# Kernel optimization log

Measured on AMD Instinct MI355X. Metric: run time of the kernel, lower is better.

## Reference

```python
import jax, jax.numpy as jnp
import numpy as np

N_SLOTS = 24   # n_slots from __init__
N_ITERS = 25   # fixed Lloyd iterations (stand-in for sklearn max_iter/convergence)
NORM_EPS = 1e-12  # torch F.normalize eps


def setup_inputs() -> dict:
    key = jax.random.key(0)
    features = jax.random.normal(key, (32, 4096, 256), dtype=jnp.float32)
    return {"features": features}


def _pairwise_sqdist(x, x_sq, centers):
    # x: [B,N,D], x_sq: [B,N,1], centers: [B,K,D] -> [B,N,K]
    c_sq = jnp.sum(centers * centers, axis=-1)  # [B,K]
    return x_sq - 2.0 * jnp.einsum('bnd,bkd->bnk', x, centers) + c_sq[:, None, :]


def _kmeans_batched(x, k, n_iters):
    # x: [B,N,D] -> centers [B,K,D], assignments [B,N]
    B, N, D = x.shape
    # deterministic init: K evenly-spaced points per batch item
    init_idx = jnp.linspace(0, N - 1, k).astype(jnp.int32)
    centers0 = x[:, init_idx, :]  # [B,K,D]
    x_sq = jnp.sum(x * x, axis=-1, keepdims=True)  # [B,N,1]

    def step(centers, _):
        d = _pairwise_sqdist(x, x_sq, centers)          # [B,N,K]
        assign = jnp.argmin(d, axis=-1)                 # [B,N]
        onehot = jax.nn.one_hot(assign, k, dtype=x.dtype)  # [B,N,K]
        counts = jnp.sum(onehot, axis=1)                # [B,K]
        sums = jnp.einsum('bnk,bnd->bkd', onehot, x)    # [B,K,D] scatter-mean numerator
        new_centers = sums / jnp.maximum(counts, 1.0)[..., None]
        # empty clusters keep their previous center
        new_centers = jnp.where(counts[..., None] > 0, new_centers, centers)
        return new_centers, None

    centers, _ = jax.lax.scan(step, centers0, None, length=n_iters)
    final_assign = jnp.argmin(_pairwise_sqdist(x, x_sq, centers), axis=-1)
    return centers, final_assign


def reference(features):
    # L2-normalize along feature dim (use_l2_normalization=True)
    norm = jnp.sqrt(jnp.sum(features * features, axis=-1, keepdims=True))
    f = features / jnp.maximum(norm, NORM_EPS)
    # original detaches before clustering (sklearn on CPU): no gradient flow
    f = jax.lax.stop_gradient(f)
    centers, assign = _kmeans_batched(f, N_SLOTS, N_ITERS)
    # slot masks: one_hot then transpose(-2,-1) -> [B, K, N] float32
    slot_masks = jax.nn.one_hot(assign, N_SLOTS, dtype=jnp.float32).transpose(0, 2, 1)
    return centers, slot_masks
```

## Files before the change

### kernel.cpp

```cpp
#include <hip/hip_runtime.h>
#include <math.h>


#define BATCH 32
#define NPTS 4096
#define DIM 256
#define NSLOT 24
#define NITER 25
#define NCH 16
#define CPTS 256

__global__ __launch_bounds__(256) void k_norm(const float* __restrict__ feat,
                                              double* __restrict__ inv_norm) {
  int lane = threadIdx.x & 63;
  int wid = threadIdx.x >> 6;
  int p = blockIdx.x * 4 + wid;
  const float4 v = *(const float4*)(feat + (size_t)p * DIM + lane * 4);
  double s = (double)v.x * v.x + (double)v.y * v.y + (double)v.z * v.z + (double)v.w * v.w;
#pragma unroll
  for (int m = 32; m; m >>= 1) s += __shfl_xor(s, m);
  if (lane == 0) inv_norm[p] = 1.0 / fmax(sqrt(s), 1e-12);
}

__device__ __forceinline__ double block_sum_256(double v, double* red) {
#pragma unroll
  for (int m = 32; m; m >>= 1) v += __shfl_xor(v, m);
  int w = threadIdx.x >> 6;
  if ((threadIdx.x & 63) == 0) red[w] = v;
  __syncthreads();
  return red[0] + red[1] + red[2] + red[3];
}

__global__ __launch_bounds__(256) void k_init_centers(const float* __restrict__ feat,
                                                      const double* __restrict__ inv_norm,
                                                      double* __restrict__ centers,
                                                      float* __restrict__ cT32,
                                                      float* __restrict__ c_sq32) {
  __shared__ double red[4];
  int t = threadIdx.x, k = blockIdx.x, b = blockIdx.y;
  int idx = (int)((double)k * (NPTS - 1) / (NSLOT - 1));
  double v = (double)feat[((size_t)b * NPTS + idx) * DIM + t] * inv_norm[b * NPTS + idx];
  centers[((size_t)b * NSLOT + k) * DIM + t] = v;
  cT32[((size_t)b * DIM + t) * NSLOT + k] = (float)v;
  double s = block_sum_256(v * v, red);
  if (t == 0) c_sq32[b * NSLOT + k] = (float)s;
}

__global__ __launch_bounds__(256) void k_transpose(const float* __restrict__ feat,
                                                   float* __restrict__ xT) {
  __shared__ float tile[64][65];
  int ix = threadIdx.x & 63, iy = threadIdx.x >> 6;
  int bx = blockIdx.x, by = blockIdx.y, b = blockIdx.z;
  const float* fb = feat + ((size_t)b * NPTS + bx * 64) * DIM + by * 64;
#pragma unroll
  for (int r = 0; r < 64; r += 4)
    tile[r + iy][ix] = fb[(size_t)(r + iy) * DIM + ix];
  __syncthreads();
  float* xb = xT + ((size_t)b * DIM + by * 64) * NPTS + bx * 64;
#pragma unroll
  for (int r = 0; r < 64; r += 4)
    xb[(size_t)(r + iy) * NPTS + ix] = tile[ix][r + iy];
}

template <bool USE_T>
__global__ __launch_bounds__(256) void k_assign(const float* __restrict__ feat,
                                                const float* __restrict__ xT,
                                                const double* __restrict__ inv_norm,
                                                const float* __restrict__ cT32,
                                                const float* __restrict__ c_sq32,
                                                int* __restrict__ assign) {
  __shared__ float part[3][64][NSLOT + 1];
  int lane = threadIdx.x & 63;
  int q = __builtin_amdgcn_readfirstlane(threadIdx.x >> 6);
  int blk = blockIdx.x, b = blockIdx.y;
  int n = blk * 64 + lane;
  const float* cb = cT32 + ((size_t)b * DIM + q * 64) * NSLOT;

  float dot[NSLOT];
#pragma unroll
  for (int k = 0; k < NSLOT; ++k) dot[k] = 0.0f;

  for (int d = 0; d < 64; d += 8) {
    float x[8];
    if (USE_T) {
      const float* xp = xT + ((size_t)b * DIM + q * 64 + d) * NPTS + n;
#pragma unroll
      for (int j = 0; j < 8; ++j) x[j] = xp[(size_t)j * NPTS];
    } else {
      float4 v = *(const float4*)(feat + ((size_t)b * NPTS + n) * DIM + q * 64 + d);
      float4 u = *(const float4*)(feat + ((size_t)b * NPTS + n) * DIM + q * 64 + d + 4);
      x[0] = v.x; x[1] = v.y; x[2] = v.z; x[3] = v.w;
      x[4] = u.x; x[5] = u.y; x[6] = u.z; x[7] = u.w;
    }
    const float* cp = cb + (size_t)d * NSLOT;
#pragma unroll
    for (int k = 0; k < NSLOT; ++k) {
      float s = dot[k];
#pragma unroll
      for (int j = 0; j < 8; ++j) s = fmaf(x[j], cp[j * NSLOT + k], s);
      dot[k] = s;
    }
  }

  if (q) {
#pragma unroll
    for (int k = 0; k < NSLOT; ++k) part[q - 1][lane][k] = dot[k];
  }
  __syncthreads();

  if (q == 0) {
    float inv = (float)inv_norm[b * NPTS + n];
    const float* csq = c_sq32 + b * NSLOT;
    int a = 0;
    float best = 0.0f;
#pragma unroll
    for (int k = 0; k < NSLOT; ++k) {
      float df = dot[k] + part[0][lane][k] + part[1][lane][k] + part[2][lane][k];
      float s = csq[k] - 2.0f * (df * inv);
      if (k == 0) { best = s; }
      else if (s < best) { best = s; a = k; }
    }
    assign[b * NPTS + n] = a;
  }
}

__global__ __launch_bounds__(256) void k_clusterS(const float* __restrict__ feat,
                                                  const double* __restrict__ inv_norm,
                                                  const int* __restrict__ assign,
                                                  double* __restrict__ psumG) {
  __shared__ double part[NSLOT * DIM];
  __shared__ int a_lds[CPTS];
  __shared__ double i_lds[CPTS];
  int t = threadIdx.x, ch = blockIdx.x, b = blockIdx.y;

  a_lds[t] = assign[b * NPTS + ch * CPTS + t];
  i_lds[t] = inv_norm[b * NPTS + ch * CPTS + t];
#pragma unroll
  for (int i = 0; i < NSLOT; ++i) part[i * DIM + t] = 0.0;
  __syncthreads();

  const float* fb = feat + ((size_t)b * NPTS + ch * CPTS) * DIM + t;
  for (int row = 0; row < CPTS; row += 4) {
    float x0 = fb[(size_t)(row + 0) * DIM];
    float x1 = fb[(size_t)(row + 1) * DIM];
    float x2 = fb[(size_t)(row + 2) * DIM];
    float x3 = fb[(size_t)(row + 3) * DIM];
    int a0 = __builtin_amdgcn_readfirstlane(a_lds[row + 0]);
    int a1 = __builtin_amdgcn_readfirstlane(a_lds[row + 1]);
    int a2 = __builtin_amdgcn_readfirstlane(a_lds[row + 2]);
    int a3 = __builtin_amdgcn_readfirstlane(a_lds[row + 3]);
    double v0 = (double)x0 * i_lds[row + 0];
    double v1 = (double)x1 * i_lds[row + 1];
    double v2 = (double)x2 * i_lds[row + 2];
    double v3 = (double)x3 * i_lds[row + 3];
    part[a0 * DIM + t] += v0;
    part[a1 * DIM + t] += v1;
    part[a2 * DIM + t] += v2;
    part[a3 * DIM + t] += v3;
  }
  __syncthreads();

  double* ps = psumG + (size_t)(b * NCH + ch) * NSLOT * DIM;
#pragma unroll
  for (int i = 0; i < NSLOT; ++i) ps[i * DIM + t] = part[i * DIM + t];
}

__global__ __launch_bounds__(256) void k_upd3(const double* __restrict__ psumG,
                                              const int* __restrict__ assign,
                                              double* __restrict__ centers,
                                              float* __restrict__ cT32,
                                              float* __restrict__ c_sq32) {
  __shared__ double red[4];
  __shared__ int scnt;
  int t = threadIdx.x, k = blockIdx.x, b = blockIdx.y;
  if (t == 0) scnt = 0;
  __syncthreads();

  double s = 0.0;
#pragma unroll
  for (int ch = 0; ch < NCH; ++ch)
    s += psumG[((size_t)(b * NCH + ch) * NSLOT + k) * DIM + t];

  int c_loc = 0;
  const int* ab = assign + b * NPTS;
#pragma unroll
  for (int j = 0; j < NPTS / 256; ++j) c_loc += (ab[t + j * 256] == k) ? 1 : 0;
#pragma unroll
  for (int m = 32; m; m >>= 1) c_loc += __shfl_xor(c_loc, m);
  if ((t & 63) == 0) atomicAdd(&scnt, c_loc);
  __syncthreads();
  int cnt = scnt;

  size_t ci = ((size_t)b * NSLOT + k) * DIM + t;
  double nc = (cnt > 0) ? (s / (double)cnt) : centers[ci];
  centers[ci] = nc;
  cT32[((size_t)b * DIM + t) * NSLOT + k] = (float)nc;
  double sq = block_sum_256(nc * nc, red);
  if (t == 0) c_sq32[b * NSLOT + k] = (float)sq;
}

__global__ __launch_bounds__(256) void k_mask(const int* __restrict__ assign,
                                              float* __restrict__ masks) {
  int t = threadIdx.x, nc = blockIdx.x, k = blockIdx.y, b = blockIdx.z;
  int n = nc * 256 + t;
  masks[((size_t)b * NSLOT + k) * NPTS + n] = (assign[b * NPTS + n] == k) ? 1.0f : 0.0f;
}

__global__ __launch_bounds__(256) void k_copyc(const double* __restrict__ centers,
                                               float* __restrict__ out_centers) {
  int t = threadIdx.x, k = blockIdx.x, b = blockIdx.y;
  size_t i = ((size_t)b * NSLOT + k) * DIM + t;
  out_centers[i] = (float)centers[i];
}

extern "C" void kernel_launch(void* const* d_in, const int* in_sizes, int n_in,
                              void* d_out, int out_size, void* d_ws, size_t ws_size,
                              hipStream_t stream) {
  (void)in_sizes; (void)n_in; (void)out_size;
  const float* feat = (const float*)d_in[0];
  float* out_centers = (float*)d_out;
  float* out_masks = out_centers + (size_t)BATCH * NSLOT * DIM;

  char* ws = (char*)d_ws;
  double* inv_norm = (double*)ws; ws += (size_t)BATCH * NPTS * 8;
  double* centers  = (double*)ws; ws += (size_t)BATCH * NSLOT * DIM * 8;
  float* cT32      = (float*)ws;  ws += (size_t)BATCH * DIM * NSLOT * 4;
  float* c_sq32    = (float*)ws;  ws += (size_t)BATCH * NSLOT * 4;
  int* assign      = (int*)ws;    ws += (size_t)BATCH * NPTS * 4;
  double* psumG    = (double*)ws; ws += (size_t)BATCH * NCH * NSLOT * DIM * 8;
  float* xT        = (float*)ws;
  size_t need_xT = (size_t)(ws - (char*)d_ws) + (size_t)BATCH * DIM * NPTS * 4;
  bool useT = ws_size >= need_xT;

  k_norm<<<BATCH * NPTS / 4, 256, 0, stream>>>(feat, inv_norm);
  k_init_centers<<<dim3(NSLOT, BATCH), 256, 0, stream>>>(feat, inv_norm, centers,
                                                         cT32, c_sq32);
  if (useT)
    k_transpose<<<dim3(NPTS / 64, DIM / 64, BATCH), 256, 0, stream>>>(feat, xT);

  for (int it = 0; it <= NITER; ++it) {
    if (useT)
      k_assign<true><<<dim3(NPTS / 64, BATCH), 256, 0, stream>>>(feat, xT, inv_norm,
                                                                 cT32, c_sq32, assign);
    else
      k_assign<false><<<dim3(NPTS / 64, BATCH), 256, 0, stream>>>(feat, xT, inv_norm,
                                                                  cT32, c_sq32, assign);
    if (it == NITER) break;
    k_clusterS<<<dim3(NCH, BATCH), 256, 0, stream>>>(feat, inv_norm, assign, psumG);
    k_upd3<<<dim3(NSLOT, BATCH), 256, 0, stream>>>(psumG, assign, centers, cT32, c_sq32);
  }

  k_mask<<<dim3(NPTS / 256, NSLOT, BATCH), 256, 0, stream>>>(assign, out_masks);
  k_copyc<<<dim3(NSLOT, BATCH), 256, 0, stream>>>(centers, out_centers);
}
```

Measured before the change: 2.047 ms.

## Fuse assignment with per-chunk cluster sums via sorted point lists

Merges the assignment and cluster-sum kernels into one kernel per 256-point chunk. Points are bucketed by assigned slot using ballots, then feature rows are summed per slot in a register double accumulator and written to per-chunk partials along with counts. The update kernel reads these counts instead of rescanning assignments, and the final pass writes masks directly. This removes the assign buffer round-trip and one launch per iteration, but uses 4x fewer blocks with each thread computing the full dot product, which lowers occupancy.

```diff
diff --git a/kernel.cpp b/kernel.cpp
--- a/kernel.cpp
+++ b/kernel.cpp
@@ -62,134 +62,153 @@
     xb[(size_t)(r + iy) * NPTS + ix] = tile[ix][r + iy];
 }
 
-template <bool USE_T>
-__global__ __launch_bounds__(256) void k_assign(const float* __restrict__ feat,
-                                                const float* __restrict__ xT,
-                                                const double* __restrict__ inv_norm,
-                                                const float* __restrict__ cT32,
-                                                const float* __restrict__ c_sq32,
-                                                int* __restrict__ assign) {
-  __shared__ float part[3][64][NSLOT + 1];
-  int lane = threadIdx.x & 63;
-  int q = __builtin_amdgcn_readfirstlane(threadIdx.x >> 6);
-  int blk = blockIdx.x, b = blockIdx.y;
-  int n = blk * 64 + lane;
-  const float* cb = cT32 + ((size_t)b * DIM + q * 64) * NSLOT;
-
-  float dot[NSLOT];
-#pragma unroll
-  for (int k = 0; k < NSLOT; ++k) dot[k] = 0.0f;
-
-  for (int d = 0; d < 64; d += 8) {
+template <bool USE_T, bool FINAL>
+__global__ __launch_bounds__(256) void k_fused(const float* __restrict__ feat,
+                                               const float* __restrict__ xT,
+                                               const double* __restrict__ inv_norm,
+                                               const float* __restrict__ cT32,
+                                               const float* __restrict__ c_sq32,
+                                               double* __restrict__ psumG,
+                                               int* __restrict__ cntG,
+                                               float* __restrict__ masks) {
+  __shared__ double i_lds[CPTS];
+  __shared__ int a_lds[CPTS];
+  __shared__ unsigned short list[CPTS];
+  __shared__ unsigned char sk_arr[CPTS];
+  __shared__ int wcnt[4][NSLOT], goff[4][NSLOT];
+  __shared__ int off_lds[NSLOT], tot_lds[NSLOT];
+  int ch = blockIdx.x, b = blockIdx.y;
+  int t = threadIdx.x;
+  int lane = t & 63;
+  int w = __builtin_amdgcn_readfirstlane(t >> 6);
+
+  i_lds[t] = inv_norm[b * NPTS + ch * CPTS + t];
+  __syncthreads();
+
+  const float* cT = cT32 + (size_t)b * DIM * NSLOT;
+  const float* csq = c_sq32 + b * NSLOT;
+  float acc[NSLOT], cur[NSLOT];
+#pragma unroll
+  for (int k = 0; k < NSLOT; ++k) acc[k] = 0.0f;
+  const float* xp = USE_T ? (xT + (size_t)b * DIM * NPTS + ch * CPTS + t)
+                          : (feat + ((size_t)b * NPTS + ch * CPTS + t) * DIM);
+  for (int q = 0; q < 4; ++q) {
+#pragma unroll
+    for (int k = 0; k < NSLOT; ++k) cur[k] = 0.0f;
+    for (int d0 = q * 64; d0 < q * 64 + 64; d0 += 8) {
+      float x[8];
+      if (USE_T) {
+#pragma unroll
+        for (int j = 0; j < 8; ++j) x[j] = xp[(size_t)(d0 + j) * NPTS];
+      } else {
+        float4 v = *(const float4*)(xp + d0);
+        float4 u = *(const float4*)(xp + d0 + 4);
+        x[0] = v.x; x[1] = v.y; x[2] = v.z; x[3] = v.w;
+        x[4] = u.x; x[5] = u.y; x[6] = u.z; x[7] = u.w;
+      }
+      const float* cp = cT + d0 * NSLOT;
+#pragma unroll
+      for (int k = 0; k < NSLOT; ++k) {
+        float s = cur[k];
+#pragma unroll
+        for (int j = 0; j < 8; ++j) s = fmaf(x[j], cp[j * NSLOT + k], s);
+        cur[k] = s;
+      }
+    }
+#pragma unroll
+    for (int k = 0; k < NSLOT; ++k) acc[k] += cur[k];
+  }
+  float inv = (float)i_lds[t];
+  int a = 0;
+  float best = 0.0f;
+#pragma unroll
+  for (int k = 0; k < NSLOT; ++k) {
+    float s = csq[k] - 2.0f * (acc[k] * inv);
+    if (k == 0) { best = s; }
+    else if (s < best) { best = s; a = k; }
+  }
+
+  if (FINAL) {
+#pragma unroll
+    for (int k = 0; k < NSLOT; ++k)
+      masks[((size_t)b * NSLOT + k) * NPTS + ch * CPTS + t] = (a == k) ? 1.0f : 0.0f;
+    return;
+  }
+  a_lds[t] = a;
+  __syncthreads();
+
+  for (int k = 0; k < NSLOT; ++k) {
+    unsigned long long bal = __ballot(a == k);
+    if (lane == 0) wcnt[w][k] = __popcll(bal);
+  }
+  __syncthreads();
+  if (t < NSLOT) {
+    tot_lds[t] = wcnt[0][t] + wcnt[1][t] + wcnt[2][t] + wcnt[3][t];
+  }
+  __syncthreads();
+  if (t < NSLOT) {
+    int off = 0;
+    for (int k2 = 0; k2 < t; ++k2) off += tot_lds[k2];
+    off_lds[t] = off;
+    int base = off;
+#pragma unroll
+    for (int g = 0; g < 4; ++g) { goff[g][t] = base; base += wcnt[g][t]; }
+    cntG[(b * NCH + ch) * NSLOT + t] = tot_lds[t];
+  }
+  __syncthreads();
+  unsigned long long lt = (1ull << lane) - 1ull;
+  for (int k = 0; k < NSLOT; ++k) {
+    unsigned long long bal = __ballot(a == k);
+    if (a == k) {
+      int pos = goff[w][k] + __popcll(bal & lt);
+      list[pos] = (unsigned short)t;
+      sk_arr[pos] = (unsigned char)k;
+    }
+  }
+  __syncthreads();
+
+  const float* fb = feat + ((size_t)b * NPTS + ch * CPTS) * DIM + t;
+  double* psB = psumG + (size_t)(b * NCH + ch) * NSLOT * DIM + t;
+  double racc = 0.0;
+  for (int i0 = 0; i0 < CPTS; i0 += 8) {
+    int nn[8];
     float x[8];
-    if (USE_T) {
-      const float* xp = xT + ((size_t)b * DIM + q * 64 + d) * NPTS + n;
-#pragma unroll
-      for (int j = 0; j < 8; ++j) x[j] = xp[(size_t)j * NPTS];
-    } else {
-      float4 v = *(const float4*)(feat + ((size_t)b * NPTS + n) * DIM + q * 64 + d);
-      float4 u = *(const float4*)(feat + ((size_t)b * NPTS + n) * DIM + q * 64 + d + 4);
-      x[0] = v.x; x[1] = v.y; x[2] = v.z; x[3] = v.w;
-      x[4] = u.x; x[5] = u.y; x[6] = u.z; x[7] = u.w;
+#pragma unroll
+    for (int j = 0; j < 8; ++j)
+      nn[j] = __builtin_amdgcn_readfirstlane((int)list[i0 + j]);
+#pragma unroll
+    for (int j = 0; j < 8; ++j) x[j] = fb[(size_t)nn[j] * DIM];
+#pragma unroll
+    for (int j = 0; j < 8; ++j) {
+      int i = i0 + j;
+      racc += (double)x[j] * i_lds[nn[j]];
+      int kcur = __builtin_amdgcn_readfirstlane((int)sk_arr[i]);
+      int knxt = (i < CPTS - 1) ? __builtin_amdgcn_readfirstlane((int)sk_arr[i + 1]) : -1;
+      if (kcur != knxt) {
+        psB[(size_t)kcur * DIM] = racc;
+        racc = 0.0;
+      }
     }
-    const float* cp = cb + (size_t)d * NSLOT;
-#pragma unroll
-    for (int k = 0; k < NSLOT; ++k) {
-      float s = dot[k];
-#pragma unroll
-      for (int j = 0; j < 8; ++j) s = fmaf(x[j], cp[j * NSLOT + k], s);
-      dot[k] = s;
-    }
-  }
-
-  if (q) {
-#pragma unroll
-    for (int k = 0; k < NSLOT; ++k) part[q - 1][lane][k] = dot[k];
-  }
-  __syncthreads();
-
-  if (q == 0) {
-    float inv = (float)inv_norm[b * NPTS + n];
-    const float* csq = c_sq32 + b * NSLOT;
-    int a = 0;
-    float best = 0.0f;
-#pragma unroll
-    for (int k = 0; k < NSLOT; ++k) {
-      float df = dot[k] + part[0][lane][k] + part[1][lane][k] + part[2][lane][k];
-      float s = csq[k] - 2.0f * (df * inv);
-      if (k == 0) { best = s; }
-      else if (s < best) { best = s; a = k; }
-    }
-    assign[b * NPTS + n] = a;
-  }
-}
-
-__global__ __launch_bounds__(256) void k_clusterS(const float* __restrict__ feat,
-                                                  const double* __restrict__ inv_norm,
-                                                  const int* __restrict__ assign,
-                                                  double* __restrict__ psumG) {
-  __shared__ double part[NSLOT * DIM];
-  __shared__ int a_lds[CPTS];
-  __shared__ double i_lds[CPTS];
-  int t = threadIdx.x, ch = blockIdx.x, b = blockIdx.y;
-
-  a_lds[t] = assign[b * NPTS + ch * CPTS + t];
-  i_lds[t] = inv_norm[b * NPTS + ch * CPTS + t];
-#pragma unroll
-  for (int i = 0; i < NSLOT; ++i) part[i * DIM + t] = 0.0;
-  __syncthreads();
-
-  const float* fb = feat + ((size_t)b * NPTS + ch * CPTS) * DIM + t;
-  for (int row = 0; row < CPTS; row += 4) {
-    float x0 = fb[(size_t)(row + 0) * DIM];
-    float x1 = fb[(size_t)(row + 1) * DIM];
-    float x2 = fb[(size_t)(row + 2) * DIM];
-    float x3 = fb[(size_t)(row + 3) * DIM];
-    int a0 = __builtin_amdgcn_readfirstlane(a_lds[row + 0]);
-    int a1 = __builtin_amdgcn_readfirstlane(a_lds[row + 1]);
-    int a2 = __builtin_amdgcn_readfirstlane(a_lds[row + 2]);
-    int a3 = __builtin_amdgcn_readfirstlane(a_lds[row + 3]);
-    double v0 = (double)x0 * i_lds[row + 0];
-    double v1 = (double)x1 * i_lds[row + 1];
-    double v2 = (double)x2 * i_lds[row + 2];
-    double v3 = (double)x3 * i_lds[row + 3];
-    part[a0 * DIM + t] += v0;
-    part[a1 * DIM + t] += v1;
-    part[a2 * DIM + t] += v2;
-    part[a3 * DIM + t] += v3;
-  }
-  __syncthreads();
-
-  double* ps = psumG + (size_t)(b * NCH + ch) * NSLOT * DIM;
-#pragma unroll
-  for (int i = 0; i < NSLOT; ++i) ps[i * DIM + t] = part[i * DIM + t];
+  }
+  for (int k = 0; k < NSLOT; ++k)
+    if (tot_lds[k] == 0) psB[(size_t)k * DIM] = 0.0;
 }
 
 __global__ __launch_bounds__(256) void k_upd3(const double* __restrict__ psumG,
-                                              const int* __restrict__ assign,
+                                              const int* __restrict__ cntG,
                                               double* __restrict__ centers,
                                               float* __restrict__ cT32,
                                               float* __restrict__ c_sq32) {
   __shared__ double red[4];
-  __shared__ int scnt;
   int t = threadIdx.x, k = blockIdx.x, b = blockIdx.y;
-  if (t == 0) scnt = 0;
-  __syncthreads();
-
   double s = 0.0;
 #pragma unroll
   for (int ch = 0; ch < NCH; ++ch)
     s += psumG[((size_t)(b * NCH + ch) * NSLOT + k) * DIM + t];
-
-  int c_loc = 0;
-  const int* ab = assign + b * NPTS;
-#pragma unroll
-  for (int j = 0; j < NPTS / 256; ++j) c_loc += (ab[t + j * 256] == k) ? 1 : 0;
-#pragma unroll
-  for (int m = 32; m; m >>= 1) c_loc += __shfl_xor(c_loc, m);
-  if ((t & 63) == 0) atomicAdd(&scnt, c_loc);
-  __syncthreads();
-  int cnt = scnt;
+  int cnt = 0;
+#pragma unroll
+  for (int ch = 0; ch < NCH; ++ch)
+    cnt += cntG[(b * NCH + ch) * NSLOT + k];
 
   size_t ci = ((size_t)b * NSLOT + k) * DIM + t;
   double nc = (cnt > 0) ? (s / (double)cnt) : centers[ci];
@@ -197,13 +216,6 @@
   cT32[((size_t)b * DIM + t) * NSLOT + k] = (float)nc;
   double sq = block_sum_256(nc * nc, red);
   if (t == 0) c_sq32[b * NSLOT + k] = (float)sq;
-}
-
-__global__ __launch_bounds__(256) void k_mask(const int* __restrict__ assign,
-                                              float* __restrict__ masks) {
-  int t = threadIdx.x, nc = blockIdx.x, k = blockIdx.y, b = blockIdx.z;
-  int n = nc * 256 + t;
-  masks[((size_t)b * NSLOT + k) * NPTS + n] = (assign[b * NPTS + n] == k) ? 1.0f : 0.0f;
 }
 
 __global__ __launch_bounds__(256) void k_copyc(const double* __restrict__ centers,
@@ -221,15 +233,15 @@
   float* out_centers = (float*)d_out;
   float* out_masks = out_centers + (size_t)BATCH * NSLOT * DIM;
 
-  char* ws = (char*)d_ws;
-  double* inv_norm = (double*)ws; ws += (size_t)BATCH * NPTS * 8;
-  double* centers  = (double*)ws; ws += (size_t)BATCH * NSLOT * DIM * 8;
-  float* cT32      = (float*)ws;  ws += (size_t)BATCH * DIM * NSLOT * 4;
-  float* c_sq32    = (float*)ws;  ws += (size_t)BATCH * NSLOT * 4;
-  int* assign      = (int*)ws;    ws += (size_t)BATCH * NPTS * 4;
-  double* psumG    = (double*)ws; ws += (size_t)BATCH * NCH * NSLOT * DIM * 8;
-  float* xT        = (float*)ws;
-  size_t need_xT = (size_t)(ws - (char*)d_ws) + (size_t)BATCH * DIM * NPTS * 4;
+  char* p = (char*)d_ws;
+  double* inv_norm = (double*)p; p += (size_t)BATCH * NPTS * 8;
+  double* centers  = (double*)p; p += (size_t)BATCH * NSLOT * DIM * 8;
+  float* cT32      = (float*)p;  p += (size_t)BATCH * DIM * NSLOT * 4;
+  float* c_sq32    = (float*)p;  p += (size_t)BATCH * NSLOT * 4;
+  double* psumG    = (double*)p; p += (size_t)BATCH * NCH * NSLOT * DIM * 8;
+  int* cntG        = (int*)p;    p += (size_t)BATCH * NCH * NSLOT * 4;
+  float* xT        = (float*)p;
+  size_t need_xT = (size_t)(p - (char*)d_ws) + (size_t)BATCH * DIM * NPTS * 4;
   bool useT = ws_size >= need_xT;
 
   k_norm<<<BATCH * NPTS / 4, 256, 0, stream>>>(feat, inv_norm);
@@ -238,18 +250,21 @@
   if (useT)
     k_transpose<<<dim3(NPTS / 64, DIM / 64, BATCH), 256, 0, stream>>>(feat, xT);
 
-  for (int it = 0; it <= NITER; ++it) {
+  dim3 fg(NCH, BATCH);
+  for (int it = 0; it < NITER; ++it) {
     if (useT)
-      k_assign<true><<<dim3(NPTS / 64, BATCH), 256, 0, stream>>>(feat, xT, inv_norm,
-                                                                 cT32, c_sq32, assign);
+      k_fused<true, false><<<fg, 256, 0, stream>>>(feat, xT, inv_norm, cT32, c_sq32,
+                                                   psumG, cntG, out_masks);
     else
-      k_assign<false><<<dim3(NPTS / 64, BATCH), 256, 0, stream>>>(feat, xT, inv_norm,
-                                                                  cT32, c_sq32, assign);
-    if (it == NITER) break;
-    k_clusterS<<<dim3(NCH, BATCH), 256, 0, stream>>>(feat, inv_norm, assign, psumG);
-    k_upd3<<<dim3(NSLOT, BATCH), 256, 0, stream>>>(psumG, assign, centers, cT32, c_sq32);
-  }
-
-  k_mask<<<dim3(NPTS / 256, NSLOT, BATCH), 256, 0, stream>>>(assign, out_masks);
+      k_fused<false, false><<<fg, 256, 0, stream>>>(feat, xT, inv_norm, cT32, c_sq32,
+                                                    psumG, cntG, out_masks);
+    k_upd3<<<dim3(NSLOT, BATCH), 256, 0, stream>>>(psumG, cntG, centers, cT32, c_sq32);
+  }
+  if (useT)
+    k_fused<true, true><<<fg, 256, 0, stream>>>(feat, xT, inv_norm, cT32, c_sq32,
+                                                psumG, cntG, out_masks);
+  else
+    k_fused<false, true><<<fg, 256, 0, stream>>>(feat, xT, inv_norm, cT32, c_sq32,
+                                                 psumG, cntG, out_masks);
   k_copyc<<<dim3(NSLOT, BATCH), 256, 0, stream>>>(centers, out_centers);
 }
```

Result: slower. 2.666 ms (+30.3%).
